# Kernel optimization log

Hardware: AMD Instinct MI355X
Metric: run time of the kernel (lower is better)

## Reference

```python
import jax, jax.numpy as jnp
import numpy as np
from jax import lax

B, T, I, H = 256, 1024, 200, 16


def setup_inputs() -> dict:
    key = jax.random.key(0)
    ks = jax.random.split(key, 11)
    s = 0.05  # small init scale for weights
    return {
        "x": jax.random.normal(ks[0], (B, T, I), dtype=jnp.float32),
        "h0": jax.random.normal(ks[1], (B, H), dtype=jnp.float32),
        "c0": jax.random.normal(ks[2], (B, H), dtype=jnp.float32),
        "W_ih": jax.random.normal(ks[3], (4 * H, I), dtype=jnp.float32) * s,
        "W_hh": jax.random.normal(ks[4], (4 * H, H), dtype=jnp.float32) * s,
        "b_ih": jax.random.normal(ks[5], (4 * H,), dtype=jnp.float32) * s,
        "b_hh": jax.random.normal(ks[6], (4 * H,), dtype=jnp.float32) * s,
        "W1": jax.random.normal(ks[7], (H, H), dtype=jnp.float32) * s,
        "b1": jax.random.normal(ks[8], (H,), dtype=jnp.float32) * s,
        "W2": jax.random.normal(ks[9], (1, H), dtype=jnp.float32) * s,
        "b2": jax.random.normal(ks[10], (1,), dtype=jnp.float32) * s,
    }


def reference(x, h0, c0, W_ih, W_hh, b_ih, b_hh, W1, b1, W2, b2):
    # Precompute input projection for all timesteps: [B, T, 4H]
    x_proj = jnp.einsum("bti,gi->btg", x, W_ih) + b_ih + b_hh

    def step(carry, xt):  # xt: [B, 4H]
        h, c = carry
        gates = xt + h @ W_hh.T
        i, f, g, o = jnp.split(gates, 4, axis=-1)  # PyTorch gate order i,f,g,o
        i = jax.nn.sigmoid(i)
        f = jax.nn.sigmoid(f)
        g = jnp.tanh(g)
        o = jax.nn.sigmoid(o)
        c = f * c + i * g
        h = o * jnp.tanh(c)
        return (h, c), h

    _, hs = lax.scan(step, (h0, c0), x_proj.transpose(1, 0, 2))  # hs: [T, B, H]
    out = hs.transpose(1, 0, 2)  # [B, T, H]
    out = jax.nn.relu(out @ W1.T + b1)          # [B, T, H]
    out = jax.nn.sigmoid(out @ W2.T + b2)       # [B, T, 1]
    return jnp.mean(out, axis=1)                # [B, 1]
```

## Files before the change

kernel.cpp:

```cpp
#include <hip/hip_runtime.h>


#define T_LEN 1024
#define NB    256
#define CHUNK 128
#define NCH   (T_LEN / CHUNK)

#define F2I(x) __float_as_int(x)
#define I2F(x) __int_as_float(x)
#define DPPF(v, ctrl) I2F(__builtin_amdgcn_update_dpp(F2I(v), F2I(v), (ctrl), 0xF, 0xF, false))
#define ROWSHL4(v) I2F(__builtin_amdgcn_update_dpp(F2I(v), F2I(v), 0x104, 0xF, 0xF, false))
#define RDLANE_I(v, l) __builtin_amdgcn_readlane((v), (l))

#define LOG2E 1.442695040888963f

typedef __bf16 bf16_t;
typedef bf16_t bf16x8 __attribute__((ext_vector_type(8)));
typedef float f32x4 __attribute__((ext_vector_type(4)));
typedef __fp16 half2_t __attribute__((ext_vector_type(2)));

#if __has_builtin(__builtin_amdgcn_exp2f)
__device__ __forceinline__ float fexp2(float x) { return __builtin_amdgcn_exp2f(x); }
#else
__device__ __forceinline__ float fexp2(float x) { return exp2f(x); }
#endif
#if __has_builtin(__builtin_amdgcn_rcpf)
__device__ __forceinline__ float frcp(float x) { return __builtin_amdgcn_rcpf(x); }
#else
__device__ __forceinline__ float frcp(float x) { return __fdividef(1.f, x); }
#endif

__device__ __forceinline__ half2_t i2h2(int x) { union { int i; half2_t h; } u; u.i = x; return u.h; }
__device__ __forceinline__ int h22i(half2_t h) { union { int i; half2_t h; } u; u.h = h; return u.i; }

#if __has_builtin(__builtin_amdgcn_fdot2)
#define FDOT2(a, b, c) __builtin_amdgcn_fdot2((a), (b), (c), false)
#else
__device__ __forceinline__ float FDOT2(half2_t a, half2_t b, float c) {
  return c + (float)a[0] * (float)b[0] + (float)a[1] * (float)b[1];
}
#endif

__device__ __forceinline__ float bf2f(unsigned short s) {
  return __uint_as_float(((unsigned int)s) << 16);
}

__global__ __launch_bounds__(256) void k0_prep(
    const float* __restrict__ Wih, const float* __restrict__ bih,
    const float* __restrict__ bhh, bf16x8* __restrict__ wB,
    float* __restrict__ biasPerm)
{
  const int idx = blockIdx.x * 256 + threadIdx.x;
  if (idx < 4 * 7 * 64) {
    const int f = idx / 448;
    const int rem = idx % 448;
    const int s = rem / 64;
    const int L = rem % 64;
    const int col = f * 16 + (L & 15);
    const int r = ((col & 3) << 4) | (col >> 2);
    const int k0 = s * 32 + (L >> 4) * 8;
    bf16x8 v;
#pragma unroll
    for (int e = 0; e < 8; ++e) {
      const int k = k0 + e;
      const float w = (k < 200) ? Wih[r * 200 + k] : 0.f;
      v[e] = (bf16_t)w;
    }
    wB[idx] = v;
  }
  if (blockIdx.x == 0 && threadIdx.x < 64) {
    const int c = threadIdx.x;
    const int r = ((c & 3) << 4) | (c >> 2);
    biasPerm[c] = bih[r] + bhh[r];
  }
}

__global__ __launch_bounds__(256) void k1_xproj(
    const float* __restrict__ x, const bf16x8* __restrict__ wB,
    const float* __restrict__ biasPerm, unsigned short* __restrict__ xproj)
{
  __shared__ bf16x8 As[4 * 7 * 64];
  __shared__ bf16x8 Bs[4 * 7 * 64];

  const int tid = threadIdx.x;
  const int L = tid & 63;
  const int w = tid >> 6;
  const long row0 = (long)blockIdx.x * 64;

  if (w == 0) {
    const unsigned short* src = (const unsigned short*)wB;
    unsigned short* dst = (unsigned short*)Bs;
#pragma unroll
    for (int it = 0; it < 28; ++it) {
      __builtin_amdgcn_global_load_lds(
          (const __attribute__((address_space(1))) unsigned int*)(src + it * 512 + L * 8),
          (__attribute__((address_space(3))) unsigned int*)(dst + it * 512),
          16, 0, 0);
    }
  }

  const float* xr = x + (row0 + w * 16 + (L & 15)) * 200;
  const int kg = (L >> 4) * 8;
#pragma unroll
  for (int s = 0; s < 7; ++s) {
    const int k0 = s * 32 + kg;
    bf16x8 v;
    if (k0 < 200) {
      float4 a = *reinterpret_cast<const float4*>(xr + k0);
      float4 b = *reinterpret_cast<const float4*>(xr + k0 + 4);
      v[0] = (bf16_t)a.x; v[1] = (bf16_t)a.y; v[2] = (bf16_t)a.z; v[3] = (bf16_t)a.w;
      v[4] = (bf16_t)b.x; v[5] = (bf16_t)b.y; v[6] = (bf16_t)b.z; v[7] = (bf16_t)b.w;
    } else {
      v[0] = (bf16_t)0.f; v[1] = (bf16_t)0.f; v[2] = (bf16_t)0.f; v[3] = (bf16_t)0.f;
      v[4] = (bf16_t)0.f; v[5] = (bf16_t)0.f; v[6] = (bf16_t)0.f; v[7] = (bf16_t)0.f;
    }
    As[(w * 7 + s) * 64 + L] = v;
  }

  __syncthreads();

  f32x4 acc0 = {0.f, 0.f, 0.f, 0.f};
  f32x4 acc1 = {0.f, 0.f, 0.f, 0.f};
  f32x4 acc2 = {0.f, 0.f, 0.f, 0.f};
  f32x4 acc3 = {0.f, 0.f, 0.f, 0.f};
#pragma unroll
  for (int s = 0; s < 7; ++s) {
    const bf16x8 a = As[(w * 7 + s) * 64 + L];
    acc0 = __builtin_amdgcn_mfma_f32_16x16x32_bf16(a, Bs[(0 * 7 + s) * 64 + L], acc0, 0, 0, 0);
    acc1 = __builtin_amdgcn_mfma_f32_16x16x32_bf16(a, Bs[(1 * 7 + s) * 64 + L], acc1, 0, 0, 0);
    acc2 = __builtin_amdgcn_mfma_f32_16x16x32_bf16(a, Bs[(2 * 7 + s) * 64 + L], acc2, 0, 0, 0);
    acc3 = __builtin_amdgcn_mfma_f32_16x16x32_bf16(a, Bs[(3 * 7 + s) * 64 + L], acc3, 0, 0, 0);
  }

  const int cb = L & 15;
  const float cs = ((cb & 3) == 2) ? (-2.f * LOG2E) : (-LOG2E);
  const long rbase = row0 + w * 16 + ((L >> 4) << 2);
  __bf16* xo = (__bf16*)xproj;
  const float bv0 = biasPerm[0 * 16 + cb];
  const float bv1 = biasPerm[1 * 16 + cb];
  const float bv2 = biasPerm[2 * 16 + cb];
  const float bv3 = biasPerm[3 * 16 + cb];
#pragma unroll
  for (int q = 0; q < 4; ++q) {
    __bf16* row = xo + (rbase + q) * 64;
    row[ 0 + cb] = (bf16_t)((acc0[q] + bv0) * cs);
    row[16 + cb] = (bf16_t)((acc1[q] + bv1) * cs);
    row[32 + cb] = (bf16_t)((acc2[q] + bv2) * cs);
    row[48 + cb] = (bf16_t)((acc3[q] + bv3) * cs);
  }
}

__device__ __forceinline__ void stage_chunk(const unsigned short* g,
                                            unsigned short* l, int lane) {
#pragma unroll
  for (int it = 0; it < 16; ++it) {
    __builtin_amdgcn_global_load_lds(
        (const __attribute__((address_space(1))) unsigned int*)(g + it * 512 + lane * 8),
        (__attribute__((address_space(3))) unsigned int*)(l + it * 512),
        16, 0, 0);
  }
}

#define PACKH(hval, d0,d1,d2,d3,d4,d5,d6,d7) do {            \
    float _hn = ROWSHL4(hval);                               \
    int _pk = h22i(__builtin_amdgcn_cvt_pkrtz((hval), _hn)); \
    d0 = RDLANE_I(_pk,  0); d1 = RDLANE_I(_pk,  8);          \
    d2 = RDLANE_I(_pk, 16); d3 = RDLANE_I(_pk, 24);          \
    d4 = RDLANE_I(_pk, 32); d5 = RDLANE_I(_pk, 40);          \
    d6 = RDLANE_I(_pk, 48); d7 = RDLANE_I(_pk, 56);          \
  } while (0)

__global__ __launch_bounds__(64, 1) void k2_scan(
    const unsigned short* __restrict__ xproj,
    const float* __restrict__ h0, const float* __restrict__ c0,
    const float* __restrict__ Whh,
    unsigned short* __restrict__ hst)
{
  __shared__ unsigned short xs[2][CHUNK * 64];
  const int b = blockIdx.x;
  const int lane = threadIdx.x;
  const int g = lane & 3;
  const int j = lane >> 2;
  const int r = (g << 4) | j;

  const unsigned short* gx = xproj + (size_t)b * (T_LEN * 64);
  stage_chunk(gx, xs[0], lane);

  const float sfac = (g == 2) ? (-2.f * LOG2E) : (-LOG2E);
  const float pfac = (g == 2) ?  2.f :  1.f;
  const float qfac = (g == 2) ? -1.f :  0.f;

  half2_t wpk[8];
#pragma unroll
  for (int q = 0; q < 4; ++q) {
    float4 w = *reinterpret_cast<const float4*>(Whh + r * 16 + q * 4);
    wpk[q * 2 + 0] = __builtin_amdgcn_cvt_pkrtz(w.x * sfac, w.y * sfac);
    wpk[q * 2 + 1] = __builtin_amdgcn_cvt_pkrtz(w.z * sfac, w.w * sfac);
  }

  float c = c0[b * 16 + j];
  float hmine = h0[b * 16 + j];
  hmine = DPPF(hmine, 0x00);

  int hp0, hp1, hp2, hp3, hp4, hp5, hp6, hp7;
  PACKH(hmine, hp0, hp1, hp2, hp3, hp4, hp5, hp6, hp7);

  unsigned short* hq = hst + (size_t)b * (T_LEN * 16) + j;

  __syncthreads();

  float buf[8];
#pragma unroll
  for (int u = 0; u < 8; ++u)
    buf[u] = bf2f(xs[0][u * 64 + lane]);

  for (int ch = 0; ch < NCH; ++ch) {
    const unsigned short* xcur = xs[ch & 1];
    if (ch + 1 < NCH) stage_chunk(gx + (ch + 1) * (CHUNK * 64),
                                  (unsigned short*)xs[(ch + 1) & 1], lane);

    for (int ts = 0; ts < CHUNK; ts += 8) {
#pragma unroll
      for (int u = 0; u < 8; ++u) {
        const float gin = buf[u];
        int tn = ts + 8 + u;
        tn = (tn < CHUNK) ? tn : (CHUNK - 1);
        buf[u] = bf2f(xcur[tn * 64 + lane]);

        float d0 = FDOT2(wpk[0], i2h2(hp0), gin);
        d0 = FDOT2(wpk[1], i2h2(hp1), d0);
        d0 = FDOT2(wpk[2], i2h2(hp2), d0);
        d0 = FDOT2(wpk[3], i2h2(hp3), d0);
        float d1 = FDOT2(wpk[4], i2h2(hp4), 0.f);
        d1 = FDOT2(wpk[5], i2h2(hp5), d1);
        d1 = FDOT2(wpk[6], i2h2(hp6), d1);
        d1 = FDOT2(wpk[7], i2h2(hp7), d1);
        float pre = d0 + d1;

        float e = fexp2(pre);
        float z = frcp(1.f + e);
        float y = fmaf(pfac, z, qfac);

        float ai = DPPF(y, 0x00);
        float af = DPPF(y, 0x55);
        float ag = DPPF(y, 0xAA);
        float ao = DPPF(y, 0xFF);

        c = fmaf(af, c, ai * ag);
        float e2 = fexp2((2.f * LOG2E) * c);
        float th = fmaf(-2.f, frcp(1.f + e2), 1.f);
        float h = ao * th;

        PACKH(h, hp0, hp1, hp2, hp3, hp4, hp5, hp6, hp7);

        bf16_t hb = (bf16_t)h;
        hq[(size_t)(ch * CHUNK + ts + u) * 16] =
            *reinterpret_cast<unsigned short*>(&hb);
      }
    }

    __syncthreads();
    if (ch + 1 < NCH) {
      const unsigned short* xn = xs[(ch + 1) & 1];
#pragma unroll
      for (int u = 0; u < 8; ++u) buf[u] = bf2f(xn[u * 64 + lane]);
    }
  }
}

__global__ __launch_bounds__(256) void k3_head(
    const unsigned short* __restrict__ hst,
    const float* __restrict__ W1, const float* __restrict__ b1,
    const float* __restrict__ W2, const float* __restrict__ b2,
    float* __restrict__ out)
{
  __shared__ float ws1[256];
  __shared__ float wsb1[16], wsw2[16];
  __shared__ float red[256];
  const int tid = threadIdx.x;
  const int b = blockIdx.x;

  ws1[tid] = W1[tid];
  if (tid < 16) { wsb1[tid] = b1[tid]; wsw2[tid] = W2[tid]; }
  __syncthreads();
  const float b2s = b2[0];

  float acc = 0.f;
#pragma unroll
  for (int it = 0; it < 4; ++it) {
    const int t = it * 256 + tid;
    const uint4* hp = reinterpret_cast<const uint4*>(hst + ((size_t)b * T_LEN + t) * 16);
    uint4 ha = hp[0], hb = hp[1];
    float h[16];
    h[0]  = bf2f((unsigned short)(ha.x & 0xffff)); h[1]  = bf2f((unsigned short)(ha.x >> 16));
    h[2]  = bf2f((unsigned short)(ha.y & 0xffff)); h[3]  = bf2f((unsigned short)(ha.y >> 16));
    h[4]  = bf2f((unsigned short)(ha.z & 0xffff)); h[5]  = bf2f((unsigned short)(ha.z >> 16));
    h[6]  = bf2f((unsigned short)(ha.w & 0xffff)); h[7]  = bf2f((unsigned short)(ha.w >> 16));
    h[8]  = bf2f((unsigned short)(hb.x & 0xffff)); h[9]  = bf2f((unsigned short)(hb.x >> 16));
    h[10] = bf2f((unsigned short)(hb.y & 0xffff)); h[11] = bf2f((unsigned short)(hb.y >> 16));
    h[12] = bf2f((unsigned short)(hb.z & 0xffff)); h[13] = bf2f((unsigned short)(hb.z >> 16));
    h[14] = bf2f((unsigned short)(hb.w & 0xffff)); h[15] = bf2f((unsigned short)(hb.w >> 16));

    float s = b2s;
#pragma unroll
    for (int jj = 0; jj < 16; ++jj) {
      float p = wsb1[jj];
#pragma unroll
      for (int k = 0; k < 16; ++k) p = fmaf(ws1[jj * 16 + k], h[k], p);
      p = fmaxf(p, 0.f);
      s = fmaf(wsw2[jj], p, s);
    }
    float e = fexp2(-LOG2E * s);
    acc += frcp(1.f + e);
  }

  red[tid] = acc;
  __syncthreads();
  if (tid < 128) red[tid] += red[tid + 128];
  __syncthreads();
  if (tid < 64) {
    float v = red[tid] + red[tid + 64];
    v += __shfl_xor(v, 32, 64);
    v += __shfl_xor(v, 16, 64);
    v += __shfl_xor(v, 8, 64);
    v += __shfl_xor(v, 4, 64);
    v += __shfl_xor(v, 2, 64);
    v += __shfl_xor(v, 1, 64);
    if (tid == 0) out[b] = v * (1.f / T_LEN);
  }
}

extern "C" void kernel_launch(void* const* d_in, const int* in_sizes, int n_in,
                              void* d_out, int out_size, void* d_ws, size_t ws_size,
                              hipStream_t stream) {
  const float* x   = (const float*)d_in[0];
  const float* h0  = (const float*)d_in[1];
  const float* c0  = (const float*)d_in[2];
  const float* Wih = (const float*)d_in[3];
  const float* Whh = (const float*)d_in[4];
  const float* bih = (const float*)d_in[5];
  const float* bhh = (const float*)d_in[6];
  const float* W1  = (const float*)d_in[7];
  const float* b1  = (const float*)d_in[8];
  const float* W2  = (const float*)d_in[9];
  const float* b2  = (const float*)d_in[10];

  char* wsb = (char*)d_ws;
  unsigned short* xproj = (unsigned short*)wsb;
  unsigned short* hst   = (unsigned short*)(wsb + 33554432);
  bf16x8* wB            = (bf16x8*)(wsb + 33554432 + 8388608);
  float* biasPerm       = (float*)(wsb + 33554432 + 8388608 + 28672);

  hipLaunchKernelGGL(k0_prep, dim3(7), dim3(256), 0, stream,
                     Wih, bih, bhh, wB, biasPerm);
  hipLaunchKernelGGL(k1_xproj, dim3(4096), dim3(256), 0, stream,
                     x, wB, biasPerm, xproj);
  hipLaunchKernelGGL(k2_scan, dim3(NB), dim3(64), 0, stream,
                     xproj, h0, c0, Whh, hst);
  hipLaunchKernelGGL(k3_head, dim3(NB), dim3(256), 0, stream,
                     hst, W1, b1, W2, b2, (float*)d_out);
}
```

Baseline: 165.1 us.

## Shorten LSTM scan critical path and store hidden states transposed with vector writes

The scan kernel now keeps the cell state pre-scaled by 2*log2e, folding that constant into the input-gate activation so the tanh exponent needs no multiply. It computes i*g with one DPP swap and multiply, and splits the 8-step dot-product chain into four shorter accumulators. Hidden states are buffered for 8 timesteps and written by one lane per unit as a 16-byte store into a [B,16,T] layout, replacing scattered 2-byte stores. The head kernel reads this transposed layout and handles two timesteps per thread. This adds register pressure and changes the rounding of the cell-state math slightly.

```diff
diff --git a/kernel.cpp b/kernel.cpp
--- a/kernel.cpp
+++ b/kernel.cpp
@@ -43,6 +43,12 @@
 
 __device__ __forceinline__ float bf2f(unsigned short s) {
   return __uint_as_float(((unsigned int)s) << 16);
+}
+__device__ __forceinline__ unsigned int pkbf(float a, float b) {
+  bf16_t x = (bf16_t)a, y = (bf16_t)b;
+  unsigned short ux, uy;
+  __builtin_memcpy(&ux, &x, 2); __builtin_memcpy(&uy, &y, 2);
+  return (unsigned int)ux | ((unsigned int)uy << 16);
 }
 
 __global__ __launch_bounds__(256) void k0_prep(
@@ -136,10 +142,10 @@
   const float cs = ((cb & 3) == 2) ? (-2.f * LOG2E) : (-LOG2E);
   const long rbase = row0 + w * 16 + ((L >> 4) << 2);
   __bf16* xo = (__bf16*)xproj;
-  const float bv0 = biasPerm[0 * 16 + cb];
-  const float bv1 = biasPerm[1 * 16 + cb];
-  const float bv2 = biasPerm[2 * 16 + cb];
-  const float bv3 = biasPerm[3 * 16 + cb];
+  const float bv0 = biasPerm[ 0 + cb];
+  const float bv1 = biasPerm[16 + cb];
+  const float bv2 = biasPerm[32 + cb];
+  const float bv3 = biasPerm[48 + cb];
 #pragma unroll
   for (int q = 0; q < 4; ++q) {
     __bf16* row = xo + (rbase + q) * 64;
@@ -187,8 +193,8 @@
   stage_chunk(gx, xs[0], lane);
 
   const float sfac = (g == 2) ? (-2.f * LOG2E) : (-LOG2E);
-  const float pfac = (g == 2) ?  2.f :  1.f;
-  const float qfac = (g == 2) ? -1.f :  0.f;
+  const float pfac = (g == 0) ? (2.f * LOG2E) : ((g == 2) ? 2.f : 1.f);
+  const float qfac = (g == 2) ? -1.f : 0.f;
 
   half2_t wpk[8];
 #pragma unroll
@@ -198,14 +204,12 @@
     wpk[q * 2 + 1] = __builtin_amdgcn_cvt_pkrtz(w.z * sfac, w.w * sfac);
   }
 
-  float c = c0[b * 16 + j];
+  float c = c0[b * 16 + j] * (2.f * LOG2E);
   float hmine = h0[b * 16 + j];
-  hmine = DPPF(hmine, 0x00);
-
   int hp0, hp1, hp2, hp3, hp4, hp5, hp6, hp7;
   PACKH(hmine, hp0, hp1, hp2, hp3, hp4, hp5, hp6, hp7);
 
-  unsigned short* hq = hst + (size_t)b * (T_LEN * 16) + j;
+  unsigned short* hq = hst + (size_t)b * (16 * T_LEN) + j * T_LEN;
 
   __syncthreads();
 
@@ -220,6 +224,7 @@
                                   (unsigned short*)xs[(ch + 1) & 1], lane);
 
     for (int ts = 0; ts < CHUNK; ts += 8) {
+      float hsv[8];
 #pragma unroll
       for (int u = 0; u < 8; ++u) {
         const float gin = buf[u];
@@ -227,35 +232,39 @@
         tn = (tn < CHUNK) ? tn : (CHUNK - 1);
         buf[u] = bf2f(xcur[tn * 64 + lane]);
 
-        float d0 = FDOT2(wpk[0], i2h2(hp0), gin);
-        d0 = FDOT2(wpk[1], i2h2(hp1), d0);
-        d0 = FDOT2(wpk[2], i2h2(hp2), d0);
-        d0 = FDOT2(wpk[3], i2h2(hp3), d0);
-        float d1 = FDOT2(wpk[4], i2h2(hp4), 0.f);
-        d1 = FDOT2(wpk[5], i2h2(hp5), d1);
-        d1 = FDOT2(wpk[6], i2h2(hp6), d1);
-        d1 = FDOT2(wpk[7], i2h2(hp7), d1);
-        float pre = d0 + d1;
+        float e0 = FDOT2(wpk[0], i2h2(hp0), gin);
+        e0 = FDOT2(wpk[1], i2h2(hp1), e0);
+        float e1 = FDOT2(wpk[2], i2h2(hp2), 0.f);
+        e1 = FDOT2(wpk[3], i2h2(hp3), e1);
+        float e2 = FDOT2(wpk[4], i2h2(hp4), 0.f);
+        e2 = FDOT2(wpk[5], i2h2(hp5), e2);
+        float e3 = FDOT2(wpk[6], i2h2(hp6), 0.f);
+        e3 = FDOT2(wpk[7], i2h2(hp7), e3);
+        float pre = (e0 + e1) + (e2 + e3);
 
         float e = fexp2(pre);
         float z = frcp(1.f + e);
         float y = fmaf(pfac, z, qfac);
 
-        float ai = DPPF(y, 0x00);
-        float af = DPPF(y, 0x55);
-        float ag = DPPF(y, 0xAA);
-        float ao = DPPF(y, 0xFF);
-
-        c = fmaf(af, c, ai * ag);
-        float e2 = fexp2((2.f * LOG2E) * c);
-        float th = fmaf(-2.f, frcp(1.f + e2), 1.f);
-        float h = ao * th;
+        float t1 = DPPF(y, 0x4E) * y;
+        float ig = DPPF(t1, 0x00);
+        c = fmaf(DPPF(y, 0x55), c, ig);
+
+        float e2x = fexp2(c);
+        float z2 = frcp(1.f + e2x);
+        float th = fmaf(-2.f, z2, 1.f);
+        float h = DPPF(y, 0xFF) * th;
 
         PACKH(h, hp0, hp1, hp2, hp3, hp4, hp5, hp6, hp7);
-
-        bf16_t hb = (bf16_t)h;
-        hq[(size_t)(ch * CHUNK + ts + u) * 16] =
-            *reinterpret_cast<unsigned short*>(&hb);
+        hsv[u] = h;
+      }
+      if (g == 0) {
+        uint4 pk;
+        pk.x = pkbf(hsv[0], hsv[1]);
+        pk.y = pkbf(hsv[2], hsv[3]);
+        pk.z = pkbf(hsv[4], hsv[5]);
+        pk.w = pkbf(hsv[6], hsv[7]);
+        *reinterpret_cast<uint4*>(hq + ch * CHUNK + ts) = pk;
       }
     }
 
@@ -285,33 +294,38 @@
   __syncthreads();
   const float b2s = b2[0];
 
+  const unsigned short* hb = hst + (size_t)b * (16 * T_LEN);
   float acc = 0.f;
 #pragma unroll
-  for (int it = 0; it < 4; ++it) {
-    const int t = it * 256 + tid;
-    const uint4* hp = reinterpret_cast<const uint4*>(hst + ((size_t)b * T_LEN + t) * 16);
-    uint4 ha = hp[0], hb = hp[1];
-    float h[16];
-    h[0]  = bf2f((unsigned short)(ha.x & 0xffff)); h[1]  = bf2f((unsigned short)(ha.x >> 16));
-    h[2]  = bf2f((unsigned short)(ha.y & 0xffff)); h[3]  = bf2f((unsigned short)(ha.y >> 16));
-    h[4]  = bf2f((unsigned short)(ha.z & 0xffff)); h[5]  = bf2f((unsigned short)(ha.z >> 16));
-    h[6]  = bf2f((unsigned short)(ha.w & 0xffff)); h[7]  = bf2f((unsigned short)(ha.w >> 16));
-    h[8]  = bf2f((unsigned short)(hb.x & 0xffff)); h[9]  = bf2f((unsigned short)(hb.x >> 16));
-    h[10] = bf2f((unsigned short)(hb.y & 0xffff)); h[11] = bf2f((unsigned short)(hb.y >> 16));
-    h[12] = bf2f((unsigned short)(hb.z & 0xffff)); h[13] = bf2f((unsigned short)(hb.z >> 16));
-    h[14] = bf2f((unsigned short)(hb.w & 0xffff)); h[15] = bf2f((unsigned short)(hb.w >> 16));
-
-    float s = b2s;
+  for (int it = 0; it < 2; ++it) {
+    const int t2 = it * 256 + tid;
+    unsigned int hp[16];
+#pragma unroll
+    for (int jj = 0; jj < 16; ++jj)
+      hp[jj] = *reinterpret_cast<const unsigned int*>(hb + jj * T_LEN + 2 * t2);
+    float h0v[16], h1v[16];
+#pragma unroll
+    for (int k = 0; k < 16; ++k) {
+      h0v[k] = bf2f((unsigned short)(hp[k] & 0xffff));
+      h1v[k] = bf2f((unsigned short)(hp[k] >> 16));
+    }
+    float s0 = b2s, s1 = b2s;
 #pragma unroll
     for (int jj = 0; jj < 16; ++jj) {
-      float p = wsb1[jj];
-#pragma unroll
-      for (int k = 0; k < 16; ++k) p = fmaf(ws1[jj * 16 + k], h[k], p);
-      p = fmaxf(p, 0.f);
-      s = fmaf(wsw2[jj], p, s);
-    }
-    float e = fexp2(-LOG2E * s);
-    acc += frcp(1.f + e);
+      float p0 = wsb1[jj], p1 = wsb1[jj];
+#pragma unroll
+      for (int k = 0; k < 16; ++k) {
+        const float wv = ws1[jj * 16 + k];
+        p0 = fmaf(wv, h0v[k], p0);
+        p1 = fmaf(wv, h1v[k], p1);
+      }
+      p0 = fmaxf(p0, 0.f);
+      p1 = fmaxf(p1, 0.f);
+      s0 = fmaf(wsw2[jj], p0, s0);
+      s1 = fmaf(wsw2[jj], p1, s1);
+    }
+    acc += frcp(1.f + fexp2(-LOG2E * s0));
+    acc += frcp(1.f + fexp2(-LOG2E * s1));
   }
 
   red[tid] = acc;
@@ -349,7 +363,7 @@
   unsigned short* xproj = (unsigned short*)wsb;
   unsigned short* hst   = (unsigned short*)(wsb + 33554432);
   bf16x8* wB            = (bf16x8*)(wsb + 33554432 + 8388608);
-  float* biasPerm       = (float*)(wsb + 33554432 + 8388608 + 28672);
+  float* biasPerm       = (float*)(wsb + 33554432 + 8388608 + 32768);
 
   hipLaunchKernelGGL(k0_prep, dim3(7), dim3(256), 0, stream,
                      Wih, bih, bhh, wB, biasPerm);
```

Result: no change. 168.1 us (+1.8%).
